# Kernel tuning notes

Hardware: AMD Instinct MI355X
Metric: run time of the kernel (lower is better)

## Reference

```python
import jax, jax.numpy as jnp
import numpy as np

N_NODES = 100000
N_EDGES = 3200000
IN_CH = 128
HID = 64


def setup_inputs() -> dict:
    key = jax.random.key(0)
    k1, k2, k3, k4 = jax.random.split(key, 4)
    x = jax.random.normal(k1, (N_NODES, IN_CH), dtype=jnp.float32)
    edge_index = jax.random.randint(k2, (2, N_EDGES), 0, N_NODES, dtype=jnp.int64)
    W1 = jax.random.normal(k3, (IN_CH, HID), dtype=jnp.float32) * (1.0 / np.sqrt(IN_CH))
    b1 = jnp.zeros((HID,), dtype=jnp.float32)
    W2 = jax.random.normal(k4, (HID, HID), dtype=jnp.float32) * (1.0 / np.sqrt(HID))
    b2 = jnp.zeros((HID,), dtype=jnp.float32)
    return {"x": x, "edge_index": edge_index, "W1": W1, "b1": b1, "W2": W2, "b2": b2}


def _gcn_conv(x, W, b, src, dst, deg_inv_sqrt, n_nodes):
    # GCNConv with self-loops and symmetric normalization:
    # out_i = sum_{j->i} d_j^-1/2 d_i^-1/2 (x_j W) + d_i^-1 (x_i W) + b
    h = x @ W                                   # [N, out]
    norm = deg_inv_sqrt[src] * deg_inv_sqrt[dst]  # [E]
    agg = jax.ops.segment_sum(h[src] * norm[:, None], dst, num_segments=n_nodes)
    agg = agg + h * (deg_inv_sqrt * deg_inv_sqrt)[:, None]  # self-loop term
    return agg + b


def reference(x, edge_index, W1, b1, W2, b2):
    n = x.shape[0]
    src, dst = edge_index[0], edge_index[1]
    # degree including self-loop
    deg = jax.ops.segment_sum(jnp.ones_like(dst, dtype=x.dtype), dst, num_segments=n) + 1.0
    deg_inv_sqrt = jax.lax.rsqrt(deg)
    h = jax.nn.relu(_gcn_conv(x, W1, b1, src, dst, deg_inv_sqrt, n))
    h = jax.nn.relu(_gcn_conv(h, W2, b2, src, dst, deg_inv_sqrt, n))
    # AdaptiveAvgPool1d(1) over the node dim -> [HID]
    return jnp.mean(h, axis=0)
```

## Files before the change

kernel.cpp:

```cpp
#include <hip/hip_runtime.h>


#define CAP 8192
#define PA_T 4096

typedef float v2f __attribute__((vector_size(8)));

__device__ __forceinline__ void acc_fp8x8(uint2 w, v2f* acc) {
    acc[0] += __builtin_amdgcn_cvt_pk_f32_fp8((int)w.x, false);
    acc[1] += __builtin_amdgcn_cvt_pk_f32_fp8((int)w.x, true);
    acc[2] += __builtin_amdgcn_cvt_pk_f32_fp8((int)w.y, false);
    acc[3] += __builtin_amdgcn_cvt_pk_f32_fp8((int)w.y, true);
}
__device__ __forceinline__ unsigned f32x4_to_fp8(float a, float b, float c, float d) {
    int w = 0;
    w = __builtin_amdgcn_cvt_pk_fp8_f32(a, b, w, false);
    w = __builtin_amdgcn_cvt_pk_fp8_f32(c, d, w, true);
    return (unsigned)w;
}

__global__ __launch_bounds__(256)
void pass_a_kernel(const int* __restrict__ src, const int* __restrict__ dst,
                   int* __restrict__ bcur, unsigned* __restrict__ keys, int e, int nb) {
    __shared__ unsigned skeys[PA_T];
    __shared__ unsigned short sbkt[PA_T];
    __shared__ int hist[1024];
    __shared__ int base[1024];
    __shared__ int curs[1024];
    __shared__ int wsum[4];

    const int tid = threadIdx.x;
    const int lane = tid & 63;
    const int wv = tid >> 6;
    const int e0 = blockIdx.x * PA_T;
    const int cnt = min(PA_T, e - e0);

    for (int i = tid; i < 1024; i += 256) hist[i] = 0;
    __syncthreads();

    for (int i = tid; i < cnt; i += 256) {
        int d = dst[e0 + i];
        atomicAdd(&hist[d >> 7], 1);
    }
    __syncthreads();

    {
        int t4 = tid * 4;
        int a0 = hist[t4], a1 = hist[t4 + 1], a2 = hist[t4 + 2], a3 = hist[t4 + 3];
        int tsum = a0 + a1 + a2 + a3;
        int inc = tsum;
        for (int off = 1; off < 64; off <<= 1) {
            int v = __shfl_up(inc, off);
            if (lane >= off) inc += v;
        }
        if (lane == 63) wsum[wv] = inc;
        __syncthreads();
        int wbase = 0;
#pragma unroll
        for (int w = 0; w < 4; ++w) wbase += (w < wv) ? wsum[w] : 0;
        int ex = wbase + inc - tsum;
        base[t4] = ex;
        base[t4 + 1] = ex + a0;
        base[t4 + 2] = ex + a0 + a1;
        base[t4 + 3] = ex + a0 + a1 + a2;
        curs[t4] = ex;
        curs[t4 + 1] = ex + a0;
        curs[t4 + 2] = ex + a0 + a1;
        curs[t4 + 3] = ex + a0 + a1 + a2;
    }
    __syncthreads();

    for (int i = tid; i < cnt; i += 256) {
        int s = src[e0 + i], d = dst[e0 + i];
        int b = d >> 7;
        int pos = atomicAdd(&curs[b], 1);
        skeys[pos] = ((unsigned)s << 7) | (unsigned)(d & 127);
        sbkt[pos] = (unsigned short)b;
    }
    __syncthreads();

    for (int b = tid; b < nb; b += 256) {
        int c = hist[b];
        int gb = c ? atomicAdd(&bcur[b], c) : 0;
        hist[b] = gb - base[b];
    }
    __syncthreads();

    for (int i = tid; i < cnt; i += 256) {
        int b = sbkt[i];
        keys[(size_t)b * CAP + hist[b] + i] = skeys[i];
    }
}

__global__ __launch_bounds__(1024)
void bscan_kernel(const int* __restrict__ bcur, int* __restrict__ bbase,
                  int* __restrict__ rowptr, int nb, int n) {
    __shared__ int lds[1024];
    int t = threadIdx.x;
    int v = (t < nb) ? bcur[t] : 0;
    lds[t] = v;
    __syncthreads();
    for (int off = 1; off < 1024; off <<= 1) {
        int a = (t >= off) ? lds[t - off] : 0;
        __syncthreads();
        lds[t] += a;
        __syncthreads();
    }
    if (t < nb) bbase[t] = lds[t] - v;
    if (t == 1023) rowptr[n] = lds[1023];
}

__global__ __launch_bounds__(256)
void bucket_csr_kernel(const unsigned* __restrict__ keys, const int* __restrict__ bcur,
                       const int* __restrict__ bbase, float* __restrict__ dis,
                       int* __restrict__ rowptr, int* __restrict__ csr_src, int n) {
    __shared__ int ssrc[CAP];
    __shared__ int hist[128];
    __shared__ int curs[128];
    __shared__ int sc[256];

    const int tid = threadIdx.x;
    const int b = blockIdx.x;
    const int v0 = b << 7;
    const int nv = min(128, n - v0);
    const int ne = bcur[b];
    const int gb = bbase[b];
    const size_t kb = (size_t)b * CAP;

    if (tid < 128) hist[tid] = 0;
    __syncthreads();
    for (int i = tid; i < ne; i += 256) atomicAdd(&hist[keys[kb + i] & 127u], 1);
    __syncthreads();

    int hv = (tid < 128) ? hist[tid] : 0;
    sc[tid] = hv;
    __syncthreads();
    for (int off = 1; off < 128; off <<= 1) {
        int a = (tid >= off) ? sc[tid - off] : 0;
        __syncthreads();
        sc[tid] += a;
        __syncthreads();
    }
    if (tid < 128) {
        int ex = sc[tid] - hv;
        curs[tid] = ex;
        if (tid < nv) {
            rowptr[v0 + tid] = gb + ex;
            dis[v0 + tid] = rsqrtf((float)hv + 1.0f);
        }
    }
    __syncthreads();

    for (int i = tid; i < ne; i += 256) {
        unsigned k = keys[kb + i];
        int pos = atomicAdd(&curs[k & 127u], 1);
        ssrc[pos] = (int)((k >> 7) << 6);
    }
    __syncthreads();

    for (int i = tid; i < ne; i += 256) csr_src[gb + i] = ssrc[i];
}

template <int K, bool FP8_IN>
__global__ __launch_bounds__(256)
void gemm_kernel(const void* __restrict__ Av, const float* __restrict__ B,
                 const float* __restrict__ dis, unsigned char* __restrict__ H, int n) {
    constexpr int KC = 64;
    constexpr int KP = KC + 4;
    __shared__ float As[64 * KP];
    __shared__ float Bs[KC * 64];
    const int tid = threadIdx.x;
    const int row0 = blockIdx.x * 64;
    const int tr = tid >> 4;
    const int tc = tid & 15;

    float acc[4][4];
#pragma unroll
    for (int j = 0; j < 4; ++j)
#pragma unroll
        for (int i = 0; i < 4; ++i) acc[j][i] = 0.f;

    for (int kc = 0; kc < K / KC; ++kc) {
        if (kc > 0) __syncthreads();
        for (int idx = tid; idx < 64 * 16; idx += 256) {
            int row = idx >> 4;
            int c4  = idx & 15;
            float4 v = make_float4(0.f, 0.f, 0.f, 0.f);
            int r = row0 + row;
            if (r < n) {
                if (FP8_IN) {
                    unsigned w = *reinterpret_cast<const unsigned*>(
                        (const unsigned char*)Av + (size_t)r * K + kc * KC + c4 * 4);
                    v2f lo = __builtin_amdgcn_cvt_pk_f32_fp8((int)w, false);
                    v2f hi = __builtin_amdgcn_cvt_pk_f32_fp8((int)w, true);
                    v = make_float4(lo[0], lo[1], hi[0], hi[1]);
                } else {
                    v = *reinterpret_cast<const float4*>(
                        (const float*)Av + (size_t)r * K + kc * KC + c4 * 4);
                }
            }
            *reinterpret_cast<float4*>(&As[row * KP + c4 * 4]) = v;
        }
        for (int idx = tid; idx < KC * 16; idx += 256) {
            int row = idx >> 4, c4 = idx & 15;
            *reinterpret_cast<float4*>(&Bs[row * 64 + c4 * 4]) =
                *reinterpret_cast<const float4*>(B + (size_t)(kc * KC + row) * 64 + c4 * 4);
        }
        __syncthreads();

#pragma unroll 2
        for (int k4 = 0; k4 < KC / 4; ++k4) {
            float4 a[4], bq[4];
#pragma unroll
            for (int j = 0; j < 4; ++j)
                a[j] = *reinterpret_cast<const float4*>(&As[(tr * 4 + j) * KP + k4 * 4]);
#pragma unroll
            for (int kk = 0; kk < 4; ++kk)
                bq[kk] = *reinterpret_cast<const float4*>(&Bs[(k4 * 4 + kk) * 64 + tc * 4]);
#pragma unroll
            for (int kk = 0; kk < 4; ++kk) {
#pragma unroll
                for (int j = 0; j < 4; ++j) {
                    float av = (kk == 0) ? a[j].x : (kk == 1) ? a[j].y : (kk == 2) ? a[j].z : a[j].w;
                    acc[j][0] = fmaf(av, bq[kk].x, acc[j][0]);
                    acc[j][1] = fmaf(av, bq[kk].y, acc[j][1]);
                    acc[j][2] = fmaf(av, bq[kk].z, acc[j][2]);
                    acc[j][3] = fmaf(av, bq[kk].w, acc[j][3]);
                }
            }
        }
    }

#pragma unroll
    for (int j = 0; j < 4; ++j) {
        int r = row0 + tr * 4 + j;
        if (r < n) {
            float ds = dis[r];
            unsigned w = f32x4_to_fp8(acc[j][0] * ds, acc[j][1] * ds,
                                      acc[j][2] * ds, acc[j][3] * ds);
            *reinterpret_cast<unsigned*>(H + (size_t)r * 64 + tc * 4) = w;
        }
    }
}

template <bool WRITE_OUT>
__global__ __launch_bounds__(256)
void agg_kernel(const int* __restrict__ rowptr, const int* __restrict__ csr_src,
                const unsigned char* __restrict__ h, const float* __restrict__ dis,
                const float* __restrict__ bias,
                unsigned char* __restrict__ out, float* __restrict__ outsum,
                int n, int zoff, float inv_n) {
    const int tid = threadIdx.x;
    const int lane = tid & 63;
    const int o = lane >> 3;
    const int cl = lane & 7;
    const int wid = blockIdx.x * 4 + (tid >> 6);
    const int nw = gridDim.x * 4;
    const int ngroups = (n + 7) >> 3;

    float bl[8];
    {
        float4 b0 = *reinterpret_cast<const float4*>(bias + cl * 8);
        float4 b1 = *reinterpret_cast<const float4*>(bias + cl * 8 + 4);
        bl[0] = b0.x; bl[1] = b0.y; bl[2] = b0.z; bl[3] = b0.w;
        bl[4] = b1.x; bl[5] = b1.y; bl[6] = b1.z; bl[7] = b1.w;
    }
    float bsum[8];
#pragma unroll
    for (int k = 0; k < 8; ++k) bsum[k] = 0.f;

    for (int g = wid; g < ngroups; g += nw) {
        const int node = g * 8 + o;
        const bool live = node < n;
        const int nc = live ? node : n - 1;
        const int rp0 = rowptr[nc];
        const int rp1 = rowptr[nc + 1];
        const int deg = live ? (rp1 - rp0) : 0;
        const float ds = dis[nc];

        v2f acc[4];
        {
            int so = live ? node * 64 : zoff;
            uint2 hw = *reinterpret_cast<const uint2*>(h + (size_t)(unsigned)so + cl * 8);
            acc[0] = __builtin_amdgcn_cvt_pk_f32_fp8((int)hw.x, false);
            acc[1] = __builtin_amdgcn_cvt_pk_f32_fp8((int)hw.x, true);
            acc[2] = __builtin_amdgcn_cvt_pk_f32_fp8((int)hw.y, false);
            acc[3] = __builtin_amdgcn_cvt_pk_f32_fp8((int)hw.y, true);
        }

        int md = deg;
        md = max(md, __shfl_xor(md, 8));
        md = max(md, __shfl_xor(md, 16));
        md = max(md, __shfl_xor(md, 32));

        if (md > 0) {
            int o0 = (0 < deg) ? csr_src[rp0]     : zoff;
            int o1 = (1 < deg) ? csr_src[rp0 + 1] : zoff;
            int o2 = (2 < deg) ? csr_src[rp0 + 2] : zoff;
            int o3 = (3 < deg) ? csr_src[rp0 + 3] : zoff;
            for (int it = 0; it < md; it += 4) {
                uint2 g0 = *reinterpret_cast<const uint2*>(h + (size_t)(unsigned)o0 + cl * 8);
                uint2 g1 = *reinterpret_cast<const uint2*>(h + (size_t)(unsigned)o1 + cl * 8);
                uint2 g2 = *reinterpret_cast<const uint2*>(h + (size_t)(unsigned)o2 + cl * 8);
                uint2 g3 = *reinterpret_cast<const uint2*>(h + (size_t)(unsigned)o3 + cl * 8);
                int c0 = csr_src[rp0 + it + 4];
                int c1 = csr_src[rp0 + it + 5];
                int c2 = csr_src[rp0 + it + 6];
                int c3 = csr_src[rp0 + it + 7];
                o0 = (it + 4 < deg) ? c0 : zoff;
                o1 = (it + 5 < deg) ? c1 : zoff;
                o2 = (it + 6 < deg) ? c2 : zoff;
                o3 = (it + 7 < deg) ? c3 : zoff;
                acc_fp8x8(g0, acc);
                acc_fp8x8(g1, acc);
                acc_fp8x8(g2, acc);
                acc_fp8x8(g3, acc);
            }
        }

        float val[8];
#pragma unroll
        for (int k = 0; k < 4; ++k) {
            val[2 * k]     = fmaxf(fmaf(acc[k][0], ds, bl[2 * k]), 0.f);
            val[2 * k + 1] = fmaxf(fmaf(acc[k][1], ds, bl[2 * k + 1]), 0.f);
        }
        if (WRITE_OUT) {
            if (live) {
                unsigned w0 = f32x4_to_fp8(val[0], val[1], val[2], val[3]);
                unsigned w1 = f32x4_to_fp8(val[4], val[5], val[6], val[7]);
                *reinterpret_cast<uint2*>(out + (size_t)node * 64 + cl * 8) = make_uint2(w0, w1);
            }
        } else {
            if (live) {
#pragma unroll
                for (int k = 0; k < 8; ++k) bsum[k] += val[k];
            }
        }
    }

    if (!WRITE_OUT) {
        __shared__ float lds[4][64];
#pragma unroll
        for (int k = 0; k < 8; ++k) {
            float v = bsum[k];
            v += __shfl_xor(v, 8);
            v += __shfl_xor(v, 16);
            v += __shfl_xor(v, 32);
            bsum[k] = v;
        }
        const int wv = tid >> 6;
        if (o == 0) {
#pragma unroll
            for (int k = 0; k < 8; ++k) lds[wv][cl * 8 + k] = bsum[k];
        }
        __syncthreads();
        if (tid < 64) {
            float s = lds[0][tid] + lds[1][tid] + lds[2][tid] + lds[3][tid];
            atomicAdd(&outsum[tid], s * inv_n);
        }
    }
}

extern "C" void kernel_launch(void* const* d_in, const int* in_sizes, int n_in,
                              void* d_out, int out_size, void* d_ws, size_t ws_size,
                              hipStream_t stream) {
    const float* x  = (const float*)d_in[0];
    const int*   ei = (const int*)d_in[1];
    const float* W1 = (const float*)d_in[2];
    const float* b1 = (const float*)d_in[3];
    const float* W2 = (const float*)d_in[4];
    const float* b2 = (const float*)d_in[5];

    const int n = in_sizes[0] / 128;
    const int e = in_sizes[1] / 2;
    const int* src = ei;
    const int* dst = ei + e;
    const int nb = (n + 127) >> 7;

    char* ws = (char*)d_ws;
    size_t off = 0;
    auto alloc = [&](size_t bytes) { void* p = ws + off; off = (off + bytes + 255) & ~(size_t)255; return p; };
    unsigned* keys = (unsigned*)alloc((size_t)nb * CAP * 4);
    int*   bcur    = (int*)  alloc((size_t)nb * 4);
    int*   bbase   = (int*)  alloc((size_t)nb * 4);
    float* dis     = (float*)alloc((size_t)n * 4);
    int*   rowptr  = (int*)  alloc((size_t)(n + 1) * 4);
    int*   csr_src = (int*)  alloc(((size_t)e + 256) * 4);
    unsigned char* bufA = (unsigned char*)alloc((size_t)(n + 1) * 64);
    unsigned char* bufB = (unsigned char*)alloc((size_t)n * 64);

    hipMemsetAsync(bcur, 0, (size_t)nb * 4, stream);
    hipMemsetAsync(d_out, 0, 64 * sizeof(float), stream);
    hipMemsetAsync(bufA + (size_t)n * 64, 0, 64, stream);

    const int pa_blocks = (e + PA_T - 1) / PA_T;
    pass_a_kernel<<<pa_blocks, 256, 0, stream>>>(src, dst, bcur, keys, e, nb);
    bscan_kernel<<<1, 1024, 0, stream>>>(bcur, bbase, rowptr, nb, n);
    bucket_csr_kernel<<<nb, 256, 0, stream>>>(keys, bcur, bbase, dis, rowptr, csr_src, n);

    const int gblocks = (n + 63) / 64;
    const int zoff = n * 64;
    const int agg_blocks = 1563;

    gemm_kernel<128, false><<<gblocks, 256, 0, stream>>>(x, W1, dis, bufA, n);
    agg_kernel<true><<<agg_blocks, 256, 0, stream>>>(rowptr, csr_src, bufA, dis, b1,
                                                     bufB, nullptr, n, zoff, 0.f);
    gemm_kernel<64, true><<<gblocks, 256, 0, stream>>>(bufB, W2, dis, bufA, n);
    agg_kernel<false><<<agg_blocks, 256, 0, stream>>>(rowptr, csr_src, bufA, dis, b2,
                                                      nullptr, (float*)d_out, n, zoff, 1.0f / (float)n);
}
```

Before: 218.2 us.

## Sort nodes by degree so aggregation wavefronts get balanced edge counts

Adds three kernels that build a degree histogram, scan it, and scatter node ids into a degree-sorted permutation. Both aggregation kernels then read nodes through this permutation, so the 8 nodes sharing a wavefront have near-equal degree. This is meant to cut the idle lanes that come from looping to the group's maximum degree. In exchange it adds three launches with global atomics, plus an extra indirection that makes rowptr, dis, self-row and output accesses non-contiguous.

```diff
diff --git a/kernel.cpp b/kernel.cpp
--- a/kernel.cpp
+++ b/kernel.cpp
@@ -159,6 +159,44 @@
     __syncthreads();
 
     for (int i = tid; i < ne; i += 256) csr_src[gb + i] = ssrc[i];
+}
+
+__global__ __launch_bounds__(256)
+void deg_hist_kernel(const int* __restrict__ rowptr, int* __restrict__ dhist, int n) {
+    int i = blockIdx.x * 256 + threadIdx.x;
+    int stride = gridDim.x * 256;
+    for (; i < n; i += stride) {
+        int d = min(rowptr[i + 1] - rowptr[i], 255);
+        atomicAdd(&dhist[d], 1);
+    }
+}
+
+__global__ __launch_bounds__(256)
+void deg_scan_kernel(const int* __restrict__ dhist, int* __restrict__ dcur) {
+    __shared__ int lds[256];
+    int t = threadIdx.x;
+    int v = dhist[t];
+    lds[t] = v;
+    __syncthreads();
+    for (int off = 1; off < 256; off <<= 1) {
+        int a = (t >= off) ? lds[t - off] : 0;
+        __syncthreads();
+        lds[t] += a;
+        __syncthreads();
+    }
+    dcur[t] = lds[t] - v;
+}
+
+__global__ __launch_bounds__(256)
+void deg_place_kernel(const int* __restrict__ rowptr, int* __restrict__ dcur,
+                      int* __restrict__ perm, int n) {
+    int i = blockIdx.x * 256 + threadIdx.x;
+    int stride = gridDim.x * 256;
+    for (; i < n; i += stride) {
+        int d = min(rowptr[i + 1] - rowptr[i], 255);
+        int pos = atomicAdd(&dcur[d], 1);
+        perm[pos] = i;
+    }
 }
 
 template <int K, bool FP8_IN>
@@ -246,6 +284,7 @@
 template <bool WRITE_OUT>
 __global__ __launch_bounds__(256)
 void agg_kernel(const int* __restrict__ rowptr, const int* __restrict__ csr_src,
+                const int* __restrict__ perm,
                 const unsigned char* __restrict__ h, const float* __restrict__ dis,
                 const float* __restrict__ bias,
                 unsigned char* __restrict__ out, float* __restrict__ outsum,
@@ -270,13 +309,12 @@
     for (int k = 0; k < 8; ++k) bsum[k] = 0.f;
 
     for (int g = wid; g < ngroups; g += nw) {
-        const int node = g * 8 + o;
-        const bool live = node < n;
-        const int nc = live ? node : n - 1;
-        const int rp0 = rowptr[nc];
-        const int rp1 = rowptr[nc + 1];
-        const int deg = live ? (rp1 - rp0) : 0;
-        const float ds = dis[nc];
+        const int pidx = g * 8 + o;
+        const bool live = pidx < n;
+        const int node = live ? perm[pidx] : (n - 1);
+        const int rp0 = rowptr[node];
+        const int deg = live ? (rowptr[node + 1] - rp0) : 0;
+        const float ds = dis[node];
 
         v2f acc[4];
         {
@@ -386,10 +424,14 @@
     float* dis     = (float*)alloc((size_t)n * 4);
     int*   rowptr  = (int*)  alloc((size_t)(n + 1) * 4);
     int*   csr_src = (int*)  alloc(((size_t)e + 256) * 4);
+    int*   dhist   = (int*)  alloc(256 * 4);
+    int*   dcur    = (int*)  alloc(256 * 4);
+    int*   perm    = (int*)  alloc((size_t)n * 4);
     unsigned char* bufA = (unsigned char*)alloc((size_t)(n + 1) * 64);
     unsigned char* bufB = (unsigned char*)alloc((size_t)n * 64);
 
     hipMemsetAsync(bcur, 0, (size_t)nb * 4, stream);
+    hipMemsetAsync(dhist, 0, 256 * 4, stream);
     hipMemsetAsync(d_out, 0, 64 * sizeof(float), stream);
     hipMemsetAsync(bufA + (size_t)n * 64, 0, 64, stream);
 
@@ -397,15 +439,18 @@
     pass_a_kernel<<<pa_blocks, 256, 0, stream>>>(src, dst, bcur, keys, e, nb);
     bscan_kernel<<<1, 1024, 0, stream>>>(bcur, bbase, rowptr, nb, n);
     bucket_csr_kernel<<<nb, 256, 0, stream>>>(keys, bcur, bbase, dis, rowptr, csr_src, n);
+    deg_hist_kernel<<<512, 256, 0, stream>>>(rowptr, dhist, n);
+    deg_scan_kernel<<<1, 256, 0, stream>>>(dhist, dcur);
+    deg_place_kernel<<<512, 256, 0, stream>>>(rowptr, dcur, perm, n);
 
     const int gblocks = (n + 63) / 64;
     const int zoff = n * 64;
     const int agg_blocks = 1563;
 
     gemm_kernel<128, false><<<gblocks, 256, 0, stream>>>(x, W1, dis, bufA, n);
-    agg_kernel<true><<<agg_blocks, 256, 0, stream>>>(rowptr, csr_src, bufA, dis, b1,
+    agg_kernel<true><<<agg_blocks, 256, 0, stream>>>(rowptr, csr_src, perm, bufA, dis, b1,
                                                      bufB, nullptr, n, zoff, 0.f);
     gemm_kernel<64, true><<<gblocks, 256, 0, stream>>>(bufB, W2, dis, bufA, n);
-    agg_kernel<false><<<agg_blocks, 256, 0, stream>>>(rowptr, csr_src, bufA, dis, b2,
+    agg_kernel<false><<<agg_blocks, 256, 0, stream>>>(rowptr, csr_src, perm, bufA, dis, b2,
                                                       nullptr, (float*)d_out, n, zoff, 1.0f / (float)n);
 }
```

After: 585.9 us. 169% more time.
